# Kernel tuning notes

Hardware: AMD Instinct MI355X
Metric: run time of the kernel (lower is better)

Reference implementation:

```python
import jax, jax.numpy as jnp
import numpy as np

# Dimensions (match init_kwargs)
N, B = 32, 16384            # num_elements (agents), batch_size
SD, AD, AD2 = 128, 64, 64   # state_dim, action_dim, action_dim2
IDIM = SD + AD              # per-agent encoder input (obs + act)
H, HEADS = 256, 4           # hidden_dim, attend_heads
AT = H // HEADS             # attend_dim = 64
ODIM = AD                   # critic output = action_dim


def setup_inputs() -> dict:
    key = jax.random.key(0)
    ks = jax.random.split(key, 20)
    g = lambda k, shape: (jax.random.normal(k, shape, jnp.float32) * 0.05)
    return {
        "agent_inputs": jax.random.normal(ks[0], (N, B, IDIM), jnp.float32),
        "state_agent": jax.random.normal(ks[1], (B, SD), jnp.float32),
        "meanfield": jax.random.normal(ks[2], (B, AD), jnp.float32),
        "meanfield2": jax.random.normal(ks[3], (B, AD2), jnp.float32),
        # per-agent critic encoders (enc_fc1)
        "enc_W": g(ks[4], (N, IDIM, H)), "enc_b": g(ks[5], (N, H)),
        # state / meanfield / meanfield2 encoders
        "sW": g(ks[6], (SD, H)), "sb": g(ks[7], (H,)),
        "mfW": g(ks[8], (AD, H)), "mfb": g(ks[9], (H,)),
        "mf2W": g(ks[10], (AD2, H)), "mf2b": g(ks[11], (H,)),
        # per-head key / selector (bias-free) and value extractors
        "Wk": g(ks[12], (HEADS, H, AT)),
        "Wsel": g(ks[13], (HEADS, H, AT)),
        "Wv": g(ks[14], (HEADS, H, AT)), "bv": g(ks[15], (HEADS, AT)),
        # critic head: Linear(4H->H) + LeakyReLU + Linear(H->odim)
        "W1": g(ks[16], (4 * H, H)), "b1": g(ks[17], (H,)),
        "W2": g(ks[18], (H, ODIM)), "b2": g(ks[19], (ODIM,)),
    }


def reference(agent_inputs, state_agent, meanfield, meanfield2,
              enc_W, enc_b, sW, sb, mfW, mfb, mf2W, mf2b,
              Wk, Wsel, Wv, bv, W1, b1, W2, b2):
    lrelu = jax.nn.leaky_relu  # default negative_slope=0.01, matches nn.LeakyReLU
    # Per-agent (obs,act) encoders: [N,B,H]
    sa = lrelu(jnp.einsum('nbi,nih->nbh', agent_inputs, enc_W) + enc_b[:, None, :])
    s_enc = lrelu(state_agent @ sW + sb)          # [B,H]
    mf_enc = lrelu(meanfield @ mfW + mfb)         # [B,H]
    mf2_enc = lrelu(meanfield2 @ mf2W + mf2b)     # [B,H]
    # agents = [0]; keys/values come from all agents except agent 0
    others = sa[1:]                               # [N-1,B,H]
    keys = jnp.einsum('nbh,ehd->enbd', others, Wk)                       # [E,N-1,B,AT]
    vals = lrelu(jnp.einsum('nbh,ehd->enbd', others, Wv) + bv[:, None, None, :])
    sel = jnp.einsum('bh,ehd->ebd', s_enc, Wsel)                         # [E,B,AT]
    logits = jnp.einsum('ebd,enbd->ebn', sel, keys) / jnp.sqrt(jnp.float32(AT))
    w = jax.nn.softmax(logits, axis=-1)                                  # over N-1 agents
    other_vals = jnp.einsum('ebn,enbd->ebd', w, vals)                    # [E,B,AT]
    # concatenate heads in order, matching torch cat over per-head results
    other_flat = jnp.transpose(other_vals, (1, 0, 2)).reshape(B, HEADS * AT)
    critic_in = jnp.concatenate([s_enc, mf_enc, mf2_enc, other_flat], axis=1)  # [B,4H]
    h1 = lrelu(critic_in @ W1 + b1)
    return h1 @ W2 + b2                                                  # all_q: [B,ODIM]
```

## Files before the change

kernel.cpp:

```cpp
#include <hip/hip_runtime.h>
#include <hip/hip_bf16.h>

#define N_AG   32
#define B_SZ   16384
#define SD_    128
#define AD_    64
#define IDIM_  192
#define H_     256
#define HEADS_ 4
#define AT_    64
#define NO_    31

typedef __attribute__((ext_vector_type(8))) short bf16x8_t;
typedef __attribute__((ext_vector_type(4))) float f32x4_t;
typedef __attribute__((ext_vector_type(4))) unsigned int u32x4_t;

__device__ inline unsigned short f2bfu(float f){
  union { __hip_bfloat16 h; unsigned short u; } cv;
  cv.h = __float2bfloat16(f);
  return cv.u;
}
__device__ inline float bflo(unsigned int u){
  union { float f; unsigned int i; } c; c.i = u << 16; return c.f;
}
__device__ inline float bfhi(unsigned int u){
  union { float f; unsigned int i; } c; c.i = u & 0xffff0000u; return c.f;
}

__device__ inline void gll16(const unsigned short* g, unsigned short* l) {
  __builtin_amdgcn_global_load_lds(
      (const __attribute__((address_space(1))) unsigned int*)g,
      (__attribute__((address_space(3))) unsigned int*)l, 16, 0, 0);
}

__device__ inline float dot8(bf16x8_t a, bf16x8_t b, float acc){
  u32x4_t au = __builtin_bit_cast(u32x4_t, a);
  u32x4_t bu = __builtin_bit_cast(u32x4_t, b);
  #pragma unroll
  for (int i = 0; i < 4; i++) {
    acc = fmaf(bflo(au[i]), bflo(bu[i]), acc);
    acc = fmaf(bfhi(au[i]), bfhi(bu[i]), acc);
  }
  return acc;
}

__global__ __launch_bounds__(256) void k_prep(
    const float* __restrict__ encW, const float* __restrict__ sW,
    const float* __restrict__ mfW,  const float* __restrict__ mf2W,
    const float* __restrict__ W1,   const float* __restrict__ W2,
    const float* __restrict__ Wv,   const float* __restrict__ Wsel,
    const float* __restrict__ Wk,
    unsigned short* __restrict__ encWt, unsigned short* __restrict__ sWt,
    unsigned short* __restrict__ mfWt,  unsigned short* __restrict__ mf2Wt,
    unsigned short* __restrict__ W1t,   unsigned short* __restrict__ W2t,
    unsigned short* __restrict__ WvT,   unsigned short* __restrict__ Mct)
{
  const int bid = blockIdx.x, tid = threadIdx.x;
  auto tr = [&](const float* src, unsigned short* dst, int K, int N, int idx){
    int kn = K * N;
    int b = idx / kn, i = idx - b * kn;
    int n = i / K, k = i - n * K;
    dst[(long)b * kn + i] = f2bfu(src[(long)b * kn + (long)k * N + n]);
  };
  if (bid < 5952)        tr(encW + 192*256, encWt, 192, 256, bid*256 + tid);
  else if (bid < 6080)   tr(sW,   sWt,  128, 256, (bid-5952)*256 + tid);
  else if (bid < 6144)   tr(mfW,  mfWt,  64, 256, (bid-6080)*256 + tid);
  else if (bid < 6208)   tr(mf2W, mf2Wt, 64, 256, (bid-6144)*256 + tid);
  else if (bid < 7232)   tr(W1,   W1t, 1024, 256, (bid-6208)*256 + tid);
  else if (bid < 7296)   tr(W2,   W2t,  256,  64, (bid-7232)*256 + tid);
  else if (bid < 7552)   tr(Wv,   WvT,  256,  64, (bid-7296)*256 + tid);
  else {
    int idx = (bid - 7552) * 256 + tid;
    int hp = idx & 255, eh = idx >> 8;
    int e = eh >> 8, h = eh & 255;
    const float* ws = Wsel + ((long)e * 256 + hp) * 64;
    const float* wk = Wk   + ((long)e * 256 + h ) * 64;
    float s = 0.f;
    #pragma unroll 8
    for (int d = 0; d < 64; d++) s += ws[d] * wk[d];
    Mct[idx] = f2bfu(0.125f * s);
  }
}

template<bool AF32, bool LRELU, bool OUTF32>
__global__ __launch_bounds__(512, 2) void k_gemm2(
    const void* __restrict__ Ap, int lda, long strideA,
    const unsigned short* __restrict__ Bt, long strideB,
    const float* __restrict__ bias, long strideBias,
    void* __restrict__ Cp, int ldc, long strideC,
    int K)
{
  __shared__ __align__(16) unsigned short Alds[2][64 * 64];
  __shared__ __align__(16) unsigned short Blds[2][256 * 64];

  const int tid = threadIdx.x;
  const int lane = tid & 63, w = tid >> 6;
  const int wr = w >> 2, wc = w & 3;
  const int lr = lane & 15, lg = lane >> 4;
  const int bm = blockIdx.x, bn = blockIdx.y, bz = blockIdx.z;

  f32x4_t acc[2][4];
  #pragma unroll
  for (int i = 0; i < 2; i++)
    #pragma unroll
    for (int j = 0; j < 4; j++) acc[i][j] = (f32x4_t){0.f, 0.f, 0.f, 0.f};

  const unsigned short* Bb = Bt + bz * strideB + (long)(bn * 256) * K;
  const int nt = K >> 6;

  auto stageB = [&](int buf, int k0){
    #pragma unroll
    for (int i = 0; i < 4; i++) {
      int c = i * 512 + tid;
      int n = c >> 3, sl = c & 7;
      gll16(Bb + (long)n * K + k0 + (((sl ^ (n & 7)) & 7) << 3), &Blds[buf][c * 8]);
    }
  };
  auto stageA = [&](int buf, int k0){
    if (AF32) {
      const float* Af = (const float*)Ap + bz * strideA + (long)(bm * 64) * lda + k0;
      #pragma unroll
      for (int i = 0; i < 2; i++) {
        int c = i * 512 + tid;
        int row = c >> 4, q = c & 15;
        float4 v = *reinterpret_cast<const float4*>(Af + (long)row * lda + q * 4);
        ushort4 u;
        u.x = f2bfu(v.x); u.y = f2bfu(v.y); u.z = f2bfu(v.z); u.w = f2bfu(v.w);
        int di = row * 64 + ((((q >> 1) ^ (row & 7)) & 7) << 3) + ((q & 1) << 2);
        *reinterpret_cast<ushort4*>(&Alds[buf][di]) = u;
      }
    } else {
      const unsigned short* Ab = (const unsigned short*)Ap + bz * strideA + (long)(bm * 64) * lda + k0;
      int row = tid >> 3, sl = tid & 7;
      gll16(Ab + (long)row * lda + (((sl ^ (row & 7)) & 7) << 3),
            &Alds[buf][tid * 8]);
    }
  };

  stageB(0, 0); stageA(0, 0);

  for (int t = 0; t < nt; t++) {
    const int cur = t & 1;
    asm volatile("s_waitcnt vmcnt(0) lgkmcnt(0)" ::: "memory");
    __builtin_amdgcn_s_barrier();
    __builtin_amdgcn_sched_barrier(0);
    if (t + 1 < nt) { stageB(cur ^ 1, (t + 1) * 64); stageA(cur ^ 1, (t + 1) * 64); }

    bf16x8_t af[2][2], bf[4][2];
    #pragma unroll
    for (int mf = 0; mf < 2; mf++)
      #pragma unroll
      for (int kk = 0; kk < 2; kk++) {
        int row = wr * 32 + mf * 16 + lr;
        af[mf][kk] = *reinterpret_cast<const bf16x8_t*>(
            &Alds[cur][row * 64 + ((((kk * 4 + lg) ^ (row & 7)) & 7) << 3)]);
      }
    #pragma unroll
    for (int nf = 0; nf < 4; nf++)
      #pragma unroll
      for (int kk = 0; kk < 2; kk++) {
        int n = wc * 64 + nf * 16 + lr;
        bf[nf][kk] = *reinterpret_cast<const bf16x8_t*>(
            &Blds[cur][n * 64 + ((((kk * 4 + lg) ^ (n & 7)) & 7) << 3)]);
      }
    #pragma unroll
    for (int kk = 0; kk < 2; kk++)
      #pragma unroll
      for (int mf = 0; mf < 2; mf++)
        #pragma unroll
        for (int nf = 0; nf < 4; nf++)
          acc[mf][nf] = __builtin_amdgcn_mfma_f32_16x16x32_bf16(af[mf][kk], bf[nf][kk], acc[mf][nf], 0, 0, 0);
  }

  const float* bp = bias ? bias + bz * strideBias : nullptr;
  #pragma unroll
  for (int nf = 0; nf < 4; nf++) {
    int col = bn * 256 + wc * 64 + nf * 16 + lr;
    float bvv = bp ? bp[col] : 0.f;
    #pragma unroll
    for (int mf = 0; mf < 2; mf++) {
      #pragma unroll
      for (int r = 0; r < 4; r++) {
        int row = bm * 64 + wr * 32 + mf * 16 + lg * 4 + r;
        float v = acc[mf][nf][r] + bvv;
        if (LRELU) v = v > 0.f ? v : 0.01f * v;
        if (OUTF32)
          ((float*)Cp)[bz * strideC + (long)row * ldc + col] = v;
        else
          ((unsigned short*)Cp)[bz * strideC + (long)row * ldc + col] = f2bfu(v);
      }
    }
  }
}

__global__ __launch_bounds__(512) void k_attnw(
    const unsigned short* __restrict__ others,
    const unsigned short* __restrict__ qbuf,
    float* __restrict__ wbuf,
    float* __restrict__ wsum)
{
  __shared__ __align__(16) unsigned short olds[2][16 * 256];

  const int tid = threadIdx.x;
  const int bm = blockIdx.x;
  const int row = tid >> 5, sub = tid & 31;
  const int e = sub >> 3, ch = sub & 7;
  const long grow = (long)bm * 16 + row;

  bf16x8_t qr[4];
  #pragma unroll
  for (int j = 0; j < 4; j++)
    qr[j] = *reinterpret_cast<const bf16x8_t*>(
        &qbuf[grow * 1024 + e * 256 + ch * 32 + j * 8]);

  float psum = 0.f;

  auto stage = [&](int buf, int n){
    int r = tid >> 5, slot = tid & 31;
    gll16(others + ((long)(bm * 16 + r) * NO_ + n) * 256 + ((slot ^ ((r & 7) << 2)) << 3),
          &olds[buf][tid * 8]);
  };

  stage(0, 0);

  for (int n = 0; n < NO_; n++) {
    const int cur = n & 1;
    __syncthreads();
    if (n + 1 < NO_) stage(cur ^ 1, n + 1);

    float d = 0.f;
    #pragma unroll
    for (int j = 0; j < 4; j++) {
      int slot = (ch * 4 + j) ^ ((row & 7) << 2);
      bf16x8_t o8 = *reinterpret_cast<const bf16x8_t*>(&olds[cur][row * 256 + slot * 8]);
      d = dot8(o8, qr[j], d);
    }
    d += __shfl_xor(d, 1);
    d += __shfl_xor(d, 2);
    d += __shfl_xor(d, 4);
    float p = __expf(d);
    psum += p;
    if (ch == 0) wbuf[grow * 124 + e * 31 + n] = p;
  }
  if (ch == 0) wsum[grow * 4 + e] = psum;
}

__global__ __launch_bounds__(512) void k_pv(
    const unsigned short* __restrict__ others,
    const unsigned short* __restrict__ WvT,
    const float* __restrict__ wbuf,
    const float* __restrict__ wsum,
    const float* __restrict__ bv,
    unsigned short* __restrict__ critic)
{
  __shared__ __align__(16) unsigned short olds[2][16 * 256];
  __shared__ float pl[2][64];

  const int tid = threadIdx.x;
  const int lane = tid & 63, w = tid >> 6;
  const int lr = lane & 15, lg = lane >> 4;
  const int bm = blockIdx.x;
  const int e = w >> 1;

  bf16x8_t wv[2][8];
  #pragma unroll
  for (int nf = 0; nf < 2; nf++)
    #pragma unroll
    for (int kk = 0; kk < 8; kk++)
      wv[nf][kk] = *reinterpret_cast<const bf16x8_t*>(
          &WvT[(long)(w * 32 + nf * 16 + lr) * 256 + kk * 32 + lg * 8]);
  float bvv[2] = { bv[w * 32 + lr], bv[w * 32 + 16 + lr] };

  f32x4_t outa[2];
  outa[0] = (f32x4_t){0.f, 0.f, 0.f, 0.f};
  outa[1] = (f32x4_t){0.f, 0.f, 0.f, 0.f};

  auto stage = [&](int buf, int n){
    int r = tid >> 5, slot = tid & 31;
    gll16(others + ((long)(bm * 16 + r) * NO_ + n) * 256 + ((slot ^ ((r & 7) << 2)) << 3),
          &olds[buf][tid * 8]);
  };
  auto stagep = [&](int buf, int n){
    if (tid < 64)
      pl[buf][tid] = wbuf[((long)bm * 16 + (tid >> 2)) * 124 + (tid & 3) * 31 + n];
  };

  stage(0, 0); stagep(0, 0);

  for (int n = 0; n < NO_; n++) {
    const int cur = n & 1;
    __syncthreads();
    if (n + 1 < NO_) { stage(cur ^ 1, n + 1); stagep(cur ^ 1, n + 1); }

    f32x4_t va[2];
    va[0] = (f32x4_t){0.f, 0.f, 0.f, 0.f};
    va[1] = (f32x4_t){0.f, 0.f, 0.f, 0.f};
    #pragma unroll
    for (int kk = 0; kk < 8; kk++) {
      bf16x8_t af = *reinterpret_cast<const bf16x8_t*>(
          &olds[cur][lr * 256 + (((kk * 4 + lg) ^ ((lr & 7) << 2)) << 3)]);
      va[0] = __builtin_amdgcn_mfma_f32_16x16x32_bf16(af, wv[0][kk], va[0], 0, 0, 0);
      va[1] = __builtin_amdgcn_mfma_f32_16x16x32_bf16(af, wv[1][kk], va[1], 0, 0, 0);
    }

    #pragma unroll
    for (int r = 0; r < 4; r++) {
      float p = pl[cur][(lg * 4 + r) * 4 + e];
      #pragma unroll
      for (int nf = 0; nf < 2; nf++) {
        float v = va[nf][r] + bvv[nf];
        v = v > 0.f ? v : 0.01f * v;
        outa[nf][r] += p * v;
      }
    }
  }

  #pragma unroll
  for (int r = 0; r < 4; r++) {
    long grow = (long)bm * 16 + lg * 4 + r;
    float inv = 1.f / wsum[grow * 4 + e];
    #pragma unroll
    for (int nf = 0; nf < 2; nf++)
      critic[grow * 1024 + 768 + w * 32 + nf * 16 + lr] = f2bfu(outa[nf][r] * inv);
  }
}

template<bool AF32, bool LRELU, bool OUTF32>
__global__ __launch_bounds__(256) void k_gemm(
    const void* __restrict__ Ap, int lda, long strideA,
    const unsigned short* __restrict__ Bt, long strideB,
    const float* __restrict__ bias, long strideBias,
    void* __restrict__ Cp, int ldc, long strideC,
    int K)
{
  __shared__ __align__(16) unsigned short Alds[128][40];
  __shared__ __align__(16) unsigned short Blds[64][40];

  const int tid = threadIdx.x;
  const int bm = blockIdx.x, bn = blockIdx.y, bz = blockIdx.z;
  const int w = tid >> 6, lane = tid & 63;
  const int wr = (w >> 1) * 64, wc = (w & 1) * 32;
  const int lr = lane & 15, lk = (lane >> 4) * 8;

  f32x4_t acc[4][2];
  #pragma unroll
  for (int i = 0; i < 4; i++)
    #pragma unroll
    for (int j = 0; j < 2; j++) acc[i][j] = (f32x4_t){0.f, 0.f, 0.f, 0.f};

  const unsigned short* Bb = Bt + bz * strideB + (long)(bn * 64) * K;

  for (int k0 = 0; k0 < K; k0 += 32) {
    if (AF32) {
      const float* A = (const float*)Ap + bz * strideA + (long)(bm * 128) * lda + k0;
      #pragma unroll
      for (int i = 0; i < 4; i++) {
        int chunk = tid + i * 256;
        int m = chunk >> 3, kc = (chunk & 7) * 4;
        const float4 v = *reinterpret_cast<const float4*>(A + (long)m * lda + kc);
        ushort4 p;
        p.x = f2bfu(v.x); p.y = f2bfu(v.y); p.z = f2bfu(v.z); p.w = f2bfu(v.w);
        *reinterpret_cast<ushort4*>(&Alds[m][kc]) = p;
      }
    } else {
      const unsigned short* A = (const unsigned short*)Ap + bz * strideA + (long)(bm * 128) * lda + k0;
      #pragma unroll
      for (int i = 0; i < 4; i++) {
        int chunk = tid + i * 256;
        int m = chunk >> 3, kc = (chunk & 7) * 4;
        *reinterpret_cast<ushort4*>(&Alds[m][kc]) =
            *reinterpret_cast<const ushort4*>(A + (long)m * lda + kc);
      }
    }
    #pragma unroll
    for (int i = 0; i < 2; i++) {
      int chunk = tid + i * 256;
      int n = chunk >> 3, kc = (chunk & 7) * 4;
      *reinterpret_cast<ushort4*>(&Blds[n][kc]) =
          *reinterpret_cast<const ushort4*>(Bb + (long)n * K + k0 + kc);
    }
    __syncthreads();

    bf16x8_t bfr0 = *reinterpret_cast<const bf16x8_t*>(&Blds[wc + lr][lk]);
    bf16x8_t bfr1 = *reinterpret_cast<const bf16x8_t*>(&Blds[wc + 16 + lr][lk]);
    #pragma unroll
    for (int mf = 0; mf < 4; mf++) {
      bf16x8_t afr = *reinterpret_cast<const bf16x8_t*>(&Alds[wr + mf * 16 + lr][lk]);
      acc[mf][0] = __builtin_amdgcn_mfma_f32_16x16x32_bf16(afr, bfr0, acc[mf][0], 0, 0, 0);
      acc[mf][1] = __builtin_amdgcn_mfma_f32_16x16x32_bf16(afr, bfr1, acc[mf][1], 0, 0, 0);
    }
    __syncthreads();
  }

  const float* bp = bias ? bias + bz * strideBias : nullptr;
  #pragma unroll
  for (int nf = 0; nf < 2; nf++) {
    int col = bn * 64 + wc + nf * 16 + lr;
    float bvv = bp ? bp[col] : 0.f;
    #pragma unroll
    for (int mf = 0; mf < 4; mf++) {
      #pragma unroll
      for (int r = 0; r < 4; r++) {
        int row = bm * 128 + wr + mf * 16 + (lane >> 4) * 4 + r;
        float v = acc[mf][nf][r] + bvv;
        if (LRELU) v = v > 0.f ? v : 0.01f * v;
        if (OUTF32)
          ((float*)Cp)[bz * strideC + (long)row * ldc + col] = v;
        else
          ((unsigned short*)Cp)[bz * strideC + (long)row * ldc + col] = f2bfu(v);
      }
    }
  }
}

extern "C" void kernel_launch(void* const* d_in, const int* in_sizes, int n_in,
                              void* d_out, int out_size, void* d_ws, size_t ws_size,
                              hipStream_t stream)
{
  (void)in_sizes; (void)n_in; (void)out_size; (void)ws_size;
  const float* agent = (const float*)d_in[0];
  const float* state = (const float*)d_in[1];
  const float* mf    = (const float*)d_in[2];
  const float* mf2   = (const float*)d_in[3];
  const float* encW  = (const float*)d_in[4];
  const float* encb  = (const float*)d_in[5];
  const float* sW    = (const float*)d_in[6];
  const float* sb    = (const float*)d_in[7];
  const float* mfW   = (const float*)d_in[8];
  const float* mfb   = (const float*)d_in[9];
  const float* mf2W  = (const float*)d_in[10];
  const float* mf2b  = (const float*)d_in[11];
  const float* Wk    = (const float*)d_in[12];
  const float* Wsel  = (const float*)d_in[13];
  const float* Wv    = (const float*)d_in[14];
  const float* bv    = (const float*)d_in[15];
  const float* W1    = (const float*)d_in[16];
  const float* b1    = (const float*)d_in[17];
  const float* W2    = (const float*)d_in[18];
  const float* b2    = (const float*)d_in[19];
  float* out = (float*)d_out;

  char* ws = (char*)d_ws;
  size_t off = 0;
  auto alloc = [&](size_t bytes) -> char* {
    char* p = ws + off; off += (bytes + 255) & ~(size_t)255; return p;
  };
  unsigned short* others = (unsigned short*)alloc((size_t)B_SZ * NO_ * H_ * 2);
  unsigned short* qbuf   = (unsigned short*)alloc((size_t)B_SZ * 1024 * 2);
  unsigned short* critic = (unsigned short*)alloc((size_t)B_SZ * 1024 * 2);
  unsigned short* h1buf  = (unsigned short*)alloc((size_t)B_SZ * H_ * 2);
  float*          wbuf   = (float*)alloc((size_t)B_SZ * HEADS_ * NO_ * 4);
  float*          wsum   = (float*)alloc((size_t)B_SZ * HEADS_ * 4);
  unsigned short* encWt  = (unsigned short*)alloc((size_t)NO_ * H_ * IDIM_ * 2);
  unsigned short* Mct    = (unsigned short*)alloc((size_t)1024 * 256 * 2);
  unsigned short* WvT    = (unsigned short*)alloc((size_t)256 * 256 * 2);
  unsigned short* sWt    = (unsigned short*)alloc((size_t)256 * 128 * 2);
  unsigned short* mfWt   = (unsigned short*)alloc((size_t)256 * 64 * 2);
  unsigned short* mf2Wt  = (unsigned short*)alloc((size_t)256 * 64 * 2);
  unsigned short* W1t    = (unsigned short*)alloc((size_t)256 * 1024 * 2);
  unsigned short* W2t    = (unsigned short*)alloc((size_t)64 * 256 * 2);

  k_prep<<<dim3(8576), 256, 0, stream>>>(
      encW, sW, mfW, mf2W, W1, W2, Wv, Wsel, Wk,
      encWt, sWt, mfWt, mf2Wt, W1t, W2t, WvT, Mct);

  k_gemm2<true, true, false><<<dim3(256, 1, NO_), 512, 0, stream>>>(
      agent + (size_t)B_SZ * IDIM_, IDIM_, (long)B_SZ * IDIM_,
      encWt, (long)H_ * IDIM_,
      encb + H_, H_,
      others, NO_ * H_, H_, IDIM_);

  k_gemm2<true, true, false><<<dim3(256, 1, 1), 512, 0, stream>>>(
      state, SD_, 0, sWt, 0, sb, 0, critic, 1024, 0, SD_);
  k_gemm2<true, true, false><<<dim3(256, 1, 1), 512, 0, stream>>>(
      mf, AD_, 0, mfWt, 0, mfb, 0, critic + 256, 1024, 0, AD_);
  k_gemm2<true, true, false><<<dim3(256, 1, 1), 512, 0, stream>>>(
      mf2, AD_, 0, mf2Wt, 0, mf2b, 0, critic + 512, 1024, 0, AD_);

  k_gemm2<false, false, false><<<dim3(256, 4, 1), 512, 0, stream>>>(
      critic, 1024, 0, Mct, 0, nullptr, 0, qbuf, 1024, 0, 256);

  k_attnw<<<dim3(B_SZ / 16), 512, 0, stream>>>(others, qbuf, wbuf, wsum);

  k_pv<<<dim3(B_SZ / 16), 512, 0, stream>>>(others, WvT, wbuf, wsum, bv, critic);

  k_gemm2<false, true, false><<<dim3(256, 1, 1), 512, 0, stream>>>(
      critic, 1024, 0, W1t, 0, b1, 0, h1buf, H_, 0, 1024);

  k_gemm<false, false, true><<<dim3(128, 1, 1), 256, 0, stream>>>(
      h1buf, H_, 0, W2t, 0, b2, 0, out, 64, 0, 256);
}
```

Before: 453.5 us.

## Fuse attention-weight and value-aggregation kernels into one pass over others

Result: slower. 472.7 us (+4.2%).

```diff
diff --git a/kernel.cpp b/kernel.cpp
--- a/kernel.cpp
+++ b/kernel.cpp
@@ -193,27 +193,44 @@
   }
 }
 
-__global__ __launch_bounds__(512) void k_attnw(
+__global__ __launch_bounds__(512) void k_attnval2(
     const unsigned short* __restrict__ others,
     const unsigned short* __restrict__ qbuf,
-    float* __restrict__ wbuf,
-    float* __restrict__ wsum)
+    const unsigned short* __restrict__ WvT,
+    const float* __restrict__ bv,
+    unsigned short* __restrict__ critic)
 {
   __shared__ __align__(16) unsigned short olds[2][16 * 256];
+  __shared__ float pbuf[64];
+  __shared__ float psbuf[64];
 
   const int tid = threadIdx.x;
+  const int lane = tid & 63, w = tid >> 6;
+  const int lr = lane & 15, lg = lane >> 4;
   const int bm = blockIdx.x;
+
   const int row = tid >> 5, sub = tid & 31;
-  const int e = sub >> 3, ch = sub & 7;
+  const int eq = sub >> 3, ch = sub & 7;
   const long grow = (long)bm * 16 + row;
-
   bf16x8_t qr[4];
   #pragma unroll
   for (int j = 0; j < 4; j++)
     qr[j] = *reinterpret_cast<const bf16x8_t*>(
-        &qbuf[grow * 1024 + e * 256 + ch * 32 + j * 8]);
-
+        &qbuf[grow * 1024 + eq * 256 + ch * 32 + j * 8]);
   float psum = 0.f;
+
+  const int e = w >> 1;
+  bf16x8_t wv[2][8];
+  #pragma unroll
+  for (int nf = 0; nf < 2; nf++)
+    #pragma unroll
+    for (int kk = 0; kk < 8; kk++)
+      wv[nf][kk] = *reinterpret_cast<const bf16x8_t*>(
+          &WvT[(long)(w * 32 + nf * 16 + lr) * 256 + kk * 32 + lg * 8]);
+  float bvv[2] = { bv[w * 32 + lr], bv[w * 32 + 16 + lr] };
+  f32x4_t outa[2];
+  outa[0] = (f32x4_t){0.f, 0.f, 0.f, 0.f};
+  outa[1] = (f32x4_t){0.f, 0.f, 0.f, 0.f};
 
   auto stage = [&](int buf, int n){
     int r = tid >> 5, slot = tid & 31;
@@ -239,58 +256,7 @@
     d += __shfl_xor(d, 2);
     d += __shfl_xor(d, 4);
     float p = __expf(d);
-    psum += p;
-    if (ch == 0) wbuf[grow * 124 + e * 31 + n] = p;
-  }
-  if (ch == 0) wsum[grow * 4 + e] = psum;
-}
-
-__global__ __launch_bounds__(512) void k_pv(
-    const unsigned short* __restrict__ others,
-    const unsigned short* __restrict__ WvT,
-    const float* __restrict__ wbuf,
-    const float* __restrict__ wsum,
-    const float* __restrict__ bv,
-    unsigned short* __restrict__ critic)
-{
-  __shared__ __align__(16) unsigned short olds[2][16 * 256];
-  __shared__ float pl[2][64];
-
-  const int tid = threadIdx.x;
-  const int lane = tid & 63, w = tid >> 6;
-  const int lr = lane & 15, lg = lane >> 4;
-  const int bm = blockIdx.x;
-  const int e = w >> 1;
-
-  bf16x8_t wv[2][8];
-  #pragma unroll
-  for (int nf = 0; nf < 2; nf++)
-    #pragma unroll
-    for (int kk = 0; kk < 8; kk++)
-      wv[nf][kk] = *reinterpret_cast<const bf16x8_t*>(
-          &WvT[(long)(w * 32 + nf * 16 + lr) * 256 + kk * 32 + lg * 8]);
-  float bvv[2] = { bv[w * 32 + lr], bv[w * 32 + 16 + lr] };
-
-  f32x4_t outa[2];
-  outa[0] = (f32x4_t){0.f, 0.f, 0.f, 0.f};
-  outa[1] = (f32x4_t){0.f, 0.f, 0.f, 0.f};
-
-  auto stage = [&](int buf, int n){
-    int r = tid >> 5, slot = tid & 31;
-    gll16(others + ((long)(bm * 16 + r) * NO_ + n) * 256 + ((slot ^ ((r & 7) << 2)) << 3),
-          &olds[buf][tid * 8]);
-  };
-  auto stagep = [&](int buf, int n){
-    if (tid < 64)
-      pl[buf][tid] = wbuf[((long)bm * 16 + (tid >> 2)) * 124 + (tid & 3) * 31 + n];
-  };
-
-  stage(0, 0); stagep(0, 0);
-
-  for (int n = 0; n < NO_; n++) {
-    const int cur = n & 1;
-    __syncthreads();
-    if (n + 1 < NO_) { stage(cur ^ 1, n + 1); stagep(cur ^ 1, n + 1); }
+    if (ch == 0) { psum += p; pbuf[row * 4 + eq] = p; }
 
     f32x4_t va[2];
     va[0] = (f32x4_t){0.f, 0.f, 0.f, 0.f};
@@ -303,25 +269,31 @@
       va[1] = __builtin_amdgcn_mfma_f32_16x16x32_bf16(af, wv[1][kk], va[1], 0, 0, 0);
     }
 
+    __syncthreads();
+
     #pragma unroll
     for (int r = 0; r < 4; r++) {
-      float p = pl[cur][(lg * 4 + r) * 4 + e];
+      float p2 = pbuf[(lg * 4 + r) * 4 + e];
       #pragma unroll
       for (int nf = 0; nf < 2; nf++) {
         float v = va[nf][r] + bvv[nf];
         v = v > 0.f ? v : 0.01f * v;
-        outa[nf][r] += p * v;
-      }
-    }
-  }
+        outa[nf][r] += p2 * v;
+      }
+    }
+  }
+
+  __syncthreads();
+  if (ch == 0) psbuf[row * 4 + eq] = psum;
+  __syncthreads();
 
   #pragma unroll
   for (int r = 0; r < 4; r++) {
-    long grow = (long)bm * 16 + lg * 4 + r;
-    float inv = 1.f / wsum[grow * 4 + e];
+    long gr = (long)bm * 16 + lg * 4 + r;
+    float inv = 1.f / psbuf[(lg * 4 + r) * 4 + e];
     #pragma unroll
     for (int nf = 0; nf < 2; nf++)
-      critic[grow * 1024 + 768 + w * 32 + nf * 16 + lr] = f2bfu(outa[nf][r] * inv);
+      critic[gr * 1024 + 768 + w * 32 + nf * 16 + lr] = f2bfu(outa[nf][r] * inv);
   }
 }
 
@@ -449,8 +421,6 @@
   unsigned short* qbuf   = (unsigned short*)alloc((size_t)B_SZ * 1024 * 2);
   unsigned short* critic = (unsigned short*)alloc((size_t)B_SZ * 1024 * 2);
   unsigned short* h1buf  = (unsigned short*)alloc((size_t)B_SZ * H_ * 2);
-  float*          wbuf   = (float*)alloc((size_t)B_SZ * HEADS_ * NO_ * 4);
-  float*          wsum   = (float*)alloc((size_t)B_SZ * HEADS_ * 4);
   unsigned short* encWt  = (unsigned short*)alloc((size_t)NO_ * H_ * IDIM_ * 2);
   unsigned short* Mct    = (unsigned short*)alloc((size_t)1024 * 256 * 2);
   unsigned short* WvT    = (unsigned short*)alloc((size_t)256 * 256 * 2);
@@ -480,9 +450,7 @@
   k_gemm2<false, false, false><<<dim3(256, 4, 1), 512, 0, stream>>>(
       critic, 1024, 0, Mct, 0, nullptr, 0, qbuf, 1024, 0, 256);
 
-  k_attnw<<<dim3(B_SZ / 16), 512, 0, stream>>>(others, qbuf, wbuf, wsum);
-
-  k_pv<<<dim3(B_SZ / 16), 512, 0, stream>>>(others, WvT, wbuf, wsum, bv, critic);
+  k_attnval2<<<dim3(B_SZ / 16), 512, 0, stream>>>(others, qbuf, WvT, bv, critic);
 
   k_gemm2<false, true, false><<<dim3(256, 1, 1), 512, 0, stream>>>(
       critic, 1024, 0, W1t, 0, b1, 0, h1buf, H_, 0, 1024);
```
